# Kernel optimization log

Hardware: AMD Instinct MI355X
Metric: run time of the kernel (lower is better)

Reference implementation:

```python
import jax, jax.numpy as jnp
import numpy as np

B, S, C = 4, 4096, 128
C4 = C // 4  # q/k channels
OUT = 128    # == in_features, required by value @ weight


def setup_inputs() -> dict:
    key = jax.random.key(0)
    ks = jax.random.split(key, 9)
    stdv = 1.0 / np.sqrt(OUT)
    u = lambda k, shape, s: jax.random.uniform(k, shape, jnp.float32, -s, s)
    kaiming = lambda k, shape: u(k, shape, float(1.0 / np.sqrt(shape[1])))
    return {
        "x": jax.random.normal(ks[0], (B, S, C), jnp.float32),
        "weight": u(ks[1], (C, OUT), stdv),      # GCN weight [in, out]
        "bias": u(ks[2], (OUT,), stdv),
        "wq": kaiming(ks[3], (C4, C)),           # conv1d k=1 == linear [out_ch, in_ch]
        "bq": u(ks[4], (C4,), float(1.0 / np.sqrt(C))),
        "wk": kaiming(ks[5], (C4, C)),
        "bk": u(ks[6], (C4,), float(1.0 / np.sqrt(C))),
        "wv": kaiming(ks[7], (OUT, C)),
        "bv": u(ks[8], (OUT,), float(1.0 / np.sqrt(C))),
    }


def reference(x, weight, bias, wq, bq, wk, bk, wv, bv):
    # conv1d with kernel_size=1 == per-position linear projection
    q = jnp.einsum("bsc,qc->bsq", x, wq) + bq        # [B,S,C4] (query, pre-permute it is [B,C4,S])
    k = jnp.einsum("bsc,qc->bsq", x, wk) + bk        # [B,S,C4]
    # scores[i,j] = key_i . query_j  (unscaled), softmax over j
    scores = jnp.einsum("bic,bjc->bij", k, q)        # [B,S,S]
    adj = jax.nn.softmax(scores, axis=-1)
    v = jnp.einsum("bsc,oc->bso", x, wv) + bv        # [B,S,OUT]
    support = jnp.einsum("bso,ou->bsu", v, weight)   # [B,S,OUT]
    out = jnp.einsum("bij,bju->biu", adj, support)   # [B,S,OUT]
    return out + bias
```

## Files before the change

### kernel.cpp

```cpp
#include <hip/hip_runtime.h>

#define NB   4
#define SEQ  4096
#define CIN  128
#define C4D  32
#define OUTC 128
#define LOG2E 1.44269504f

typedef __attribute__((ext_vector_type(8))) short bf16x8;
typedef __attribute__((ext_vector_type(4))) float f32x4;

__device__ __forceinline__ short f2bf(float f) {
  union { float f; unsigned u; } v; v.f = f;
  unsigned r = v.u + 0x7FFFu + ((v.u >> 16) & 1u);
  return (short)(r >> 16);
}

__device__ __forceinline__ unsigned cvt_pk_bf16(float lo, float hi) {
  unsigned r;
  asm("v_cvt_pk_bf16_f32 %0, %1, %2" : "=v"(r) : "v"(lo), "v"(hi));
  return r;
}

__device__ __forceinline__ float fast_exp2(float x) {
  float r;
  asm("v_exp_f32 %0, %1" : "=v"(r) : "v"(x));
  return r;
}

__device__ __forceinline__ f32x4 mfma16(bf16x8 a, bf16x8 b, f32x4 c) {
  return __builtin_amdgcn_mfma_f32_16x16x32_bf16(a, b, c, 0, 0, 0);
}

__global__ void k_fuse(const float* __restrict__ wq, const float* __restrict__ wk,
                       const float* __restrict__ wv, const float* __restrict__ weight,
                       const float* __restrict__ bv,
                       short* __restrict__ wqb, short* __restrict__ wkb,
                       short* __restrict__ wfT, float* __restrict__ bfu) {
  int u = blockIdx.x, c = threadIdx.x;
  float a0 = 0.f, a1 = 0.f, a2 = 0.f, a3 = 0.f;
  for (int o = 0; o < OUTC; o += 4) {
    a0 += wv[(o + 0) * CIN + c] * weight[(o + 0) * OUTC + u];
    a1 += wv[(o + 1) * CIN + c] * weight[(o + 1) * OUTC + u];
    a2 += wv[(o + 2) * CIN + c] * weight[(o + 2) * OUTC + u];
    a3 += wv[(o + 3) * CIN + c] * weight[(o + 3) * OUTC + u];
  }
  wfT[u * CIN + c] = f2bf((a0 + a1) + (a2 + a3));
  if (u < C4D) {
    wqb[u * CIN + c] = f2bf(wq[u * CIN + c]);
    wkb[u * CIN + c] = f2bf(wk[u * CIN + c]);
  }
  if (c == 0) {
    float b0 = 0.f, b1 = 0.f;
    for (int o = 0; o < OUTC; o += 2) {
      b0 += bv[o] * weight[o * OUTC + u];
      b1 += bv[o + 1] * weight[(o + 1) * OUTC + u];
    }
    bfu[u] = b0 + b1;
  }
}

__device__ __forceinline__ int wswz(int byte) {
  return byte ^ (((byte >> 8) & 7) << 4);
}

__global__ __launch_bounds__(256) void k_proj(
    const float* __restrict__ x, const float* __restrict__ bq, const float* __restrict__ bk,
    const short* __restrict__ wall, const float* __restrict__ bfu,
    short* __restrict__ ql, short* __restrict__ kb, short* __restrict__ vfb) {
  const int tid = threadIdx.x;
  const int wid = tid >> 6, lane = tid & 63;
  const int lo = lane & 15, g = lane >> 4;
  const int p0 = blockIdx.x * 64 + wid * 16;

  __shared__ __align__(16) short WL[24576];
#pragma unroll
  for (int i = 0; i < 12; ++i) {
    bf16x8 v = *(const bf16x8*)(wall + i * 2048 + tid * 8);
    *(bf16x8*)((char*)WL + wswz((i * 2048 + tid * 8) * 2)) = v;
  }
  __syncthreads();

  auto wfrag = [&](int idx) -> bf16x8 {
    return *(const bf16x8*)((char*)WL + wswz(idx * 2));
  };

  f32x4 aq[2] = {}, ak[2] = {}, as_[8] = {};

#pragma unroll
  for (int kk = 0; kk < 4; ++kk) {
    const float* xp = x + (size_t)(p0 + lo) * CIN + kk * 32 + g * 8;
    float4 xa = *(const float4*)xp;
    float4 xb = *(const float4*)(xp + 4);
    bf16x8 af;
    af[0] = f2bf(xa.x); af[1] = f2bf(xa.y); af[2] = f2bf(xa.z); af[3] = f2bf(xa.w);
    af[4] = f2bf(xb.x); af[5] = f2bf(xb.y); af[6] = f2bf(xb.z); af[7] = f2bf(xb.w);
#pragma unroll
    for (int n = 0; n < 2; ++n) {
      bf16x8 bq_ = wfrag((n * 16 + lo) * CIN + kk * 32 + g * 8);
      aq[n] = mfma16(af, bq_, aq[n]);
      bf16x8 bk_ = wfrag(4096 + (n * 16 + lo) * CIN + kk * 32 + g * 8);
      ak[n] = mfma16(af, bk_, ak[n]);
    }
#pragma unroll
    for (int n = 0; n < 8; ++n) {
      bf16x8 bs = wfrag(8192 + (n * 16 + lo) * CIN + kk * 32 + g * 8);
      as_[n] = mfma16(af, bs, as_[n]);
    }
  }

#pragma unroll
  for (int n = 0; n < 2; ++n) {
    float bqv = bq[n * 16 + lo], bkv = bk[n * 16 + lo];
    int u = n * 16 + lo;
#pragma unroll
    for (int r = 0; r < 4; ++r) {
      int p = p0 + 4 * g + r;
      int bb = p >> 12, s = p & (SEQ - 1);
      ql[(size_t)bb * (SEQ * 32) + (size_t)(s >> 5) * 1024 + ((s >> 4) & 1) * 512 +
         (u >> 3) * 128 + (s & 15) * 8 + (u & 7)] = f2bf(aq[n][r] + bqv);
      kb[(size_t)p * C4D + u] = f2bf((ak[n][r] + bkv) * LOG2E);
    }
  }
  {
    const int p = p0 + 4 * g;
    const int bb = p >> 12, s = p & (SEQ - 1);
#pragma unroll
    for (int n = 0; n < 8; ++n) {
      int u = n * 16 + lo;
      float bvv = bfu[u];
      uint2 w;
      w.x = cvt_pk_bf16(as_[n][0] + bvv, as_[n][1] + bvv);
      w.y = cvt_pk_bf16(as_[n][2] + bvv, as_[n][3] + bvv);
      *(uint2*)&vfb[(size_t)bb * (SEQ * 128) + (size_t)(s >> 5) * 4096 + (u >> 4) * 512 +
                    ((s >> 2) & 3) * 128 + (u & 15) * 8 + ((s >> 4) & 1) * 4] = w;
    }
  }
}

__global__ __launch_bounds__(256, 3) void k_attn(
    const short* __restrict__ ql, const short* __restrict__ kb,
    const short* __restrict__ vfb, const float* __restrict__ bias,
    float* __restrict__ out) {
  const int tid = threadIdx.x;
  const int wid = tid >> 6, lane = tid & 63;
  const int lo = lane & 15, g = lane >> 4;
  const int bid = blockIdx.x;
  const int xb = ((bid & 7) << 6) | (bid >> 3);
  const int b = xb >> 7;
  const int iw = (xb & 127) * 32;

  __shared__ float OS[2][4096];
  __shared__ float OL[2][512];
  __shared__ float MS[2][32];

  const short* qB = ql + (size_t)b * (SEQ * 32) + (size_t)wid * 32768;
  const short* vB = vfb + (size_t)b * (SEQ * 128) + (size_t)wid * 131072;

  bf16x8 kf[2];
#pragma unroll
  for (int c = 0; c < 2; ++c)
    kf[c] = *(const bf16x8*)(kb + (size_t)(b * SEQ + iw + 16 * c + lo) * C4D + g * 8);

  f32x4 o[2][8];
#pragma unroll
  for (int c = 0; c < 2; ++c)
#pragma unroll
    for (int n = 0; n < 8; ++n) o[c][n] = (f32x4){0.f, 0.f, 0.f, 0.f};
  f32x4 olv[2];
  olv[0] = (f32x4){0.f, 0.f, 0.f, 0.f};
  olv[1] = (f32x4){0.f, 0.f, 0.f, 0.f};

  float ma[2];
  const f32x4 zf = {0.f, 0.f, 0.f, 0.f};
  bf16x8 ones;
#pragma unroll
  for (int e = 0; e < 8; ++e) ones[e] = (short)0x3F80;

  bf16x8 pf[2];

  bf16x8 qf0 = *(const bf16x8*)(qB + lane * 8);
  bf16x8 qf1 = *(const bf16x8*)(qB + 512 + lane * 8);

  {
    bf16x8 vfr[8];
#pragma unroll
    for (int n = 0; n < 8; ++n)
      vfr[n] = *(const bf16x8*)(vB + n * 512 + lane * 8);

    f32x4 s0[2], s1[2];
    __builtin_amdgcn_s_setprio(1);
#pragma unroll
    for (int c = 0; c < 2; ++c) {
      s0[c] = mfma16(qf0, kf[c], zf);
      s1[c] = mfma16(qf1, kf[c], zf);
    }
    __builtin_amdgcn_s_setprio(0);

    qf0 = *(const bf16x8*)(qB + 1024 + lane * 8);
    qf1 = *(const bf16x8*)(qB + 1536 + lane * 8);

#pragma unroll
    for (int c = 0; c < 2; ++c) {
      float tm = fmaxf(fmaxf(fmaxf(s0[c][0], s0[c][1]), fmaxf(s0[c][2], s0[c][3])),
                       fmaxf(fmaxf(s1[c][0], s1[c][1]), fmaxf(s1[c][2], s1[c][3])));
      tm = fmaxf(tm, __shfl_xor(tm, 16, 64));
      tm = fmaxf(tm, __shfl_xor(tm, 32, 64));
      ma[c] = tm;
    }

#pragma unroll
    for (int c = 0; c < 2; ++c) {
      float p[8];
#pragma unroll
      for (int r = 0; r < 4; ++r) {
        p[r]     = fast_exp2(s0[c][r] - ma[c]);
        p[4 + r] = fast_exp2(s1[c][r] - ma[c]);
      }
      union { bf16x8 v8; unsigned u[4]; } pk;
      pk.u[0] = cvt_pk_bf16(p[0], p[1]);
      pk.u[1] = cvt_pk_bf16(p[2], p[3]);
      pk.u[2] = cvt_pk_bf16(p[4], p[5]);
      pk.u[3] = cvt_pk_bf16(p[6], p[7]);
      pf[c] = pk.v8;
    }

    __builtin_amdgcn_s_setprio(1);
#pragma unroll
    for (int n = 0; n < 8; ++n) {
      o[0][n] = mfma16(pf[0], vfr[n], o[0][n]);
      o[1][n] = mfma16(pf[1], vfr[n], o[1][n]);
    }
    olv[0] = mfma16(pf[0], ones, olv[0]);
    olv[1] = mfma16(pf[1], ones, olv[1]);
    __builtin_amdgcn_s_setprio(0);
  }

  for (int t = 1; t < 32; ++t) {
    bf16x8 vfr[8];
    const short* vt = vB + (size_t)t * 4096;
#pragma unroll
    for (int n = 0; n < 8; ++n)
      vfr[n] = *(const bf16x8*)(vt + n * 512 + lane * 8);

    f32x4 s0[2], s1[2];
    __builtin_amdgcn_s_setprio(1);
#pragma unroll
    for (int c = 0; c < 2; ++c) {
      s0[c] = mfma16(qf0, kf[c], zf);
      s1[c] = mfma16(qf1, kf[c], zf);
    }
    __builtin_amdgcn_s_setprio(0);

    if (t + 1 < 32) {
      const short* qt = qB + (size_t)(t + 1) * 1024;
      qf0 = *(const bf16x8*)(qt + lane * 8);
      qf1 = *(const bf16x8*)(qt + 512 + lane * 8);
    }

#pragma unroll
    for (int c = 0; c < 2; ++c) {
      float p[8];
#pragma unroll
      for (int r = 0; r < 4; ++r) {
        p[r]     = fast_exp2(s0[c][r] - ma[c]);
        p[4 + r] = fast_exp2(s1[c][r] - ma[c]);
      }
      union { bf16x8 v8; unsigned u[4]; } pk;
      pk.u[0] = cvt_pk_bf16(p[0], p[1]);
      pk.u[1] = cvt_pk_bf16(p[2], p[3]);
      pk.u[2] = cvt_pk_bf16(p[4], p[5]);
      pk.u[3] = cvt_pk_bf16(p[6], p[7]);
      pf[c] = pk.v8;
    }

    __builtin_amdgcn_s_setprio(1);
#pragma unroll
    for (int n = 0; n < 8; ++n) {
      o[0][n] = mfma16(pf[0], vfr[n], o[0][n]);
      o[1][n] = mfma16(pf[1], vfr[n], o[1][n]);
    }
    olv[0] = mfma16(pf[0], ones, olv[0]);
    olv[1] = mfma16(pf[1], ones, olv[1]);
    __builtin_amdgcn_s_setprio(0);
  }

  auto write_slot = [&](int s) {
#pragma unroll
    for (int c = 0; c < 2; ++c)
#pragma unroll
      for (int n = 0; n < 8; ++n)
        *(f32x4*)&OS[s][(c * 8 + n) * 256 + lane * 4] = o[c][n];
#pragma unroll
    for (int c = 0; c < 2; ++c)
      *(f32x4*)&OL[s][c * 256 + lane * 4] = olv[c];
    if (lane < 16) {
#pragma unroll
      for (int c = 0; c < 2; ++c) MS[s][c * 16 + lo] = ma[c];
    }
  };
  auto merge_slot = [&](int s) {
#pragma unroll
    for (int c = 0; c < 2; ++c) {
      float ms = MS[s][c * 16 + lo];
      float M = fmaxf(ma[c], ms);
      float eo = fast_exp2(ma[c] - M), es = fast_exp2(ms - M);
      ma[c] = M;
      float eor[4], esr[4];
#pragma unroll
      for (int r = 0; r < 4; ++r) {
        eor[r] = __shfl(eo, 4 * g + r, 64);
        esr[r] = __shfl(es, 4 * g + r, 64);
      }
#pragma unroll
      for (int n = 0; n < 8; ++n) {
        f32x4 v = *(f32x4*)&OS[s][(c * 8 + n) * 256 + lane * 4];
#pragma unroll
        for (int r = 0; r < 4; ++r)
          o[c][n][r] = eor[r] * o[c][n][r] + esr[r] * v[r];
      }
      f32x4 vl = *(f32x4*)&OL[s][c * 256 + lane * 4];
#pragma unroll
      for (int r = 0; r < 4; ++r)
        olv[c][r] = eor[r] * olv[c][r] + esr[r] * vl[r];
    }
  };

  if (wid == 1) write_slot(0);
  if (wid == 3) write_slot(1);
  __syncthreads();
  if (wid == 0) merge_slot(0);
  if (wid == 2) merge_slot(1);
  __syncthreads();
  if (wid == 2) write_slot(0);
  __syncthreads();
  if (wid == 0) {
    merge_slot(0);
    float* outp = out + (size_t)(b * SEQ + iw) * OUTC;
#pragma unroll
    for (int c = 0; c < 2; ++c) {
      float lir[4];
#pragma unroll
      for (int r = 0; r < 4; ++r) lir[r] = 1.f / olv[c][r];
#pragma unroll
      for (int n = 0; n < 8; ++n) {
        float bu = bias[n * 16 + lo];
#pragma unroll
        for (int r = 0; r < 4; ++r)
          outp[(size_t)(c * 16 + 4 * g + r) * OUTC + n * 16 + lo] =
              o[c][n][r] * lir[r] + bu;
      }
    }
  }
}

extern "C" void kernel_launch(void* const* d_in, const int* in_sizes, int n_in,
                              void* d_out, int out_size, void* d_ws, size_t ws_size,
                              hipStream_t stream) {
  (void)in_sizes; (void)n_in; (void)out_size; (void)ws_size;
  const float* x      = (const float*)d_in[0];
  const float* weight = (const float*)d_in[1];
  const float* bias   = (const float*)d_in[2];
  const float* wq     = (const float*)d_in[3];
  const float* bq     = (const float*)d_in[4];
  const float* wk     = (const float*)d_in[5];
  const float* bk     = (const float*)d_in[6];
  const float* wv     = (const float*)d_in[7];
  const float* bv     = (const float*)d_in[8];
  float* out = (float*)d_out;

  char* ws = (char*)d_ws;
  short* kbuf = (short*)(ws);
  short* vfb  = (short*)(ws + ((size_t)1 << 20));
  short* qlb  = (short*)(ws + ((size_t)5 << 20));
  short* wqb  = (short*)(ws + ((size_t)6 << 20));
  short* wkb  = (short*)(ws + ((size_t)6 << 20) + 8192);
  short* wfT  = (short*)(ws + ((size_t)6 << 20) + 16384);
  float* bfu  = (float*)(ws + ((size_t)6 << 20) + 49152);

  hipLaunchKernelGGL(k_fuse, dim3(OUTC), dim3(CIN), 0, stream,
                     wq, wk, wv, weight, bv, wqb, wkb, wfT, bfu);
  hipLaunchKernelGGL(k_proj, dim3(NB * SEQ / 64), dim3(256), 0, stream,
                     x, bq, bk, wqb , bfu, qlb, kbuf, vfb);
  hipLaunchKernelGGL(k_attn, dim3(NB * SEQ / 32), dim3(256), 0, stream,
                     qlb, kbuf, vfb, bias, out);
}
```

Measured before the change: 49.33 us.

## Split attention KV tiles across six waves per block with three-way merge

Raises the attention block from 4 to 6 waves. The 128 key/value tiles per batch are now split into uneven chunks of 22 or 21 tiles, so each wave runs a shorter serial loop, and the partial results are combined through a deeper shared-memory merge tree with a third slot. The V-fragment loads are also split into two halves, with the second half issued after the score MFMAs, to overlap loads with compute. In exchange it uses more LDS per block and adds merge steps, and the larger block size with the same launch-bounds occupancy hint may tighten the register budget.

```diff
diff --git a/kernel.cpp b/kernel.cpp
--- a/kernel.cpp
+++ b/kernel.cpp
@@ -138,7 +138,7 @@
   }
 }
 
-__global__ __launch_bounds__(256, 3) void k_attn(
+__global__ __launch_bounds__(384, 3) void k_attn(
     const short* __restrict__ ql, const short* __restrict__ kb,
     const short* __restrict__ vfb, const float* __restrict__ bias,
     float* __restrict__ out) {
@@ -150,12 +150,15 @@
   const int b = xb >> 7;
   const int iw = (xb & 127) * 32;
 
-  __shared__ float OS[2][4096];
-  __shared__ float OL[2][512];
-  __shared__ float MS[2][32];
-
-  const short* qB = ql + (size_t)b * (SEQ * 32) + (size_t)wid * 32768;
-  const short* vB = vfb + (size_t)b * (SEQ * 128) + (size_t)wid * 131072;
+  __shared__ float OS[3][4096];
+  __shared__ float OL[3][512];
+  __shared__ float MS[3][32];
+
+  const int ntile = (wid < 2) ? 22 : 21;
+  const int tbase = wid * 21 + (wid < 2 ? wid : 2);
+
+  const short* qB = ql + (size_t)b * (SEQ * 32) + (size_t)tbase * 1024;
+  const short* vB = vfb + (size_t)b * (SEQ * 128) + (size_t)tbase * 4096;
 
   bf16x8 kf[2];
 #pragma unroll
@@ -183,10 +186,10 @@
   bf16x8 qf1 = *(const bf16x8*)(qB + 512 + lane * 8);
 
   {
-    bf16x8 vfr[8];
-#pragma unroll
-    for (int n = 0; n < 8; ++n)
-      vfr[n] = *(const bf16x8*)(vB + n * 512 + lane * 8);
+    bf16x8 va[4];
+#pragma unroll
+    for (int n = 0; n < 4; ++n)
+      va[n] = *(const bf16x8*)(vB + n * 512 + lane * 8);
 
     f32x4 s0[2], s1[2];
     __builtin_amdgcn_s_setprio(1);
@@ -196,6 +199,11 @@
       s1[c] = mfma16(qf1, kf[c], zf);
     }
     __builtin_amdgcn_s_setprio(0);
+
+    bf16x8 vb_[4];
+#pragma unroll
+    for (int n = 0; n < 4; ++n)
+      vb_[n] = *(const bf16x8*)(vB + (4 + n) * 512 + lane * 8);
 
     qf0 = *(const bf16x8*)(qB + 1024 + lane * 8);
     qf1 = *(const bf16x8*)(qB + 1536 + lane * 8);
@@ -227,21 +235,26 @@
 
     __builtin_amdgcn_s_setprio(1);
 #pragma unroll
-    for (int n = 0; n < 8; ++n) {
-      o[0][n] = mfma16(pf[0], vfr[n], o[0][n]);
-      o[1][n] = mfma16(pf[1], vfr[n], o[1][n]);
+    for (int n = 0; n < 4; ++n) {
+      o[0][n] = mfma16(pf[0], va[n], o[0][n]);
+      o[1][n] = mfma16(pf[1], va[n], o[1][n]);
+    }
+#pragma unroll
+    for (int n = 0; n < 4; ++n) {
+      o[0][4 + n] = mfma16(pf[0], vb_[n], o[0][4 + n]);
+      o[1][4 + n] = mfma16(pf[1], vb_[n], o[1][4 + n]);
     }
     olv[0] = mfma16(pf[0], ones, olv[0]);
     olv[1] = mfma16(pf[1], ones, olv[1]);
     __builtin_amdgcn_s_setprio(0);
   }
 
-  for (int t = 1; t < 32; ++t) {
-    bf16x8 vfr[8];
+  for (int t = 1; t < ntile; ++t) {
     const short* vt = vB + (size_t)t * 4096;
-#pragma unroll
-    for (int n = 0; n < 8; ++n)
-      vfr[n] = *(const bf16x8*)(vt + n * 512 + lane * 8);
+    bf16x8 va[4];
+#pragma unroll
+    for (int n = 0; n < 4; ++n)
+      va[n] = *(const bf16x8*)(vt + n * 512 + lane * 8);
 
     f32x4 s0[2], s1[2];
     __builtin_amdgcn_s_setprio(1);
@@ -252,7 +265,12 @@
     }
     __builtin_amdgcn_s_setprio(0);
 
-    if (t + 1 < 32) {
+    bf16x8 vb_[4];
+#pragma unroll
+    for (int n = 0; n < 4; ++n)
+      vb_[n] = *(const bf16x8*)(vt + (4 + n) * 512 + lane * 8);
+
+    if (t + 1 < ntile) {
       const short* qt = qB + (size_t)(t + 1) * 1024;
       qf0 = *(const bf16x8*)(qt + lane * 8);
       qf1 = *(const bf16x8*)(qt + 512 + lane * 8);
@@ -276,9 +294,14 @@
 
     __builtin_amdgcn_s_setprio(1);
 #pragma unroll
-    for (int n = 0; n < 8; ++n) {
-      o[0][n] = mfma16(pf[0], vfr[n], o[0][n]);
-      o[1][n] = mfma16(pf[1], vfr[n], o[1][n]);
+    for (int n = 0; n < 4; ++n) {
+      o[0][n] = mfma16(pf[0], va[n], o[0][n]);
+      o[1][n] = mfma16(pf[1], va[n], o[1][n]);
+    }
+#pragma unroll
+    for (int n = 0; n < 4; ++n) {
+      o[0][4 + n] = mfma16(pf[0], vb_[n], o[0][4 + n]);
+      o[1][4 + n] = mfma16(pf[1], vb_[n], o[1][4 + n]);
     }
     olv[0] = mfma16(pf[0], ones, olv[0]);
     olv[1] = mfma16(pf[1], ones, olv[1]);
@@ -328,14 +351,18 @@
 
   if (wid == 1) write_slot(0);
   if (wid == 3) write_slot(1);
+  if (wid == 5) write_slot(2);
   __syncthreads();
   if (wid == 0) merge_slot(0);
   if (wid == 2) merge_slot(1);
+  if (wid == 4) merge_slot(2);
   __syncthreads();
   if (wid == 2) write_slot(0);
+  if (wid == 4) write_slot(1);
   __syncthreads();
   if (wid == 0) {
     merge_slot(0);
+    merge_slot(1);
     float* outp = out + (size_t)(b * SEQ + iw) * OUTC;
 #pragma unroll
     for (int c = 0; c < 2; ++c) {
@@ -382,6 +409,6 @@
                      wq, wk, wv, weight, bv, wqb, wkb, wfT, bfu);
   hipLaunchKernelGGL(k_proj, dim3(NB * SEQ / 64), dim3(256), 0, stream,
                      x, bq, bk, wqb , bfu, qlb, kbuf, vfb);
-  hipLaunchKernelGGL(k_attn, dim3(NB * SEQ / 32), dim3(256), 0, stream,
+  hipLaunchKernelGGL(k_attn, dim3(NB * SEQ / 32), dim3(384), 0, stream,
                      qlb, kbuf, vfb, bias, out);
 }
```

Result: slower. 52.50 us (+6.4%).
